# Kernel tuning notes

Hardware: AMD Instinct MI355X
Metric: run time of the kernel (lower is better)

Reference implementation:

```python
import jax, jax.numpy as jnp
import numpy as np

K = 16            # top-k negatives kept per row
TEMP = 0.01       # softmax temperature
V = 0.95          # geometric decay base
NEG_FILL = -1e9   # masks out same-class entries before topk (never selected since k << #negatives)


def _l2norm(x):
    # torch F.normalize: x / max(||x||, eps)
    n = jnp.linalg.norm(x, axis=-1, keepdims=True)
    return x / jnp.maximum(n, 1e-12)


def setup_inputs() -> dict:
    key = jax.random.key(0)
    k1, k2, k3 = jax.random.split(key, 3)
    feature = jax.random.normal(k1, (4096, 128), dtype=jnp.float32)
    negative_features = jax.random.normal(k2, (4, 4096, 128), dtype=jnp.float32)
    target = jax.random.randint(k3, (4096,), 0, 4)
    return {"feature": feature, "target": target,
            "negative_features": negative_features, "idx": 0}


def reference(feature, target, negative_features, idx):
    J = negative_features.shape[0]
    f = _l2norm(feature)                       # [n, d]
    negs = _l2norm(negative_features)          # [J, n, d]
    # cosine similarity for every negative set: [J, n, n]
    sims = jnp.einsum('nd,jmd->jnm', f, negs)
    # same-class mask, applied only to the idx-th set
    same = target[:, None] == target[None, :]  # [n, n]
    sims = sims.at[idx].set(jnp.where(same, NEG_FILL, sims[idx]))
    # per-row top-k over the last (candidate) dim: [J, n, K]
    top, _ = jax.lax.top_k(sims, K)
    logits = jnp.transpose(top, (1, 0, 2)) / TEMP   # [n, J, K]
    p = jax.nn.softmax(logits, axis=1)
    logp = jax.nn.log_softmax(logits, axis=1)
    ent = jnp.sum(p * logp, axis=1)                 # [n, K]
    decay = V ** jnp.arange(K, dtype=jnp.float32)
    decay = decay / jnp.sum(decay)                  # L1-normalized, matches F.normalize(p=1)
    loss = jnp.mean(jnp.sum(ent * decay, axis=1)) + jnp.log(jnp.float32(J))
    return loss
```

## Files before the change

kernel.cpp:

```cpp
#include <hip/hip_runtime.h>
#include <hip/hip_bf16.h>
#include <math.h>

#define N 4096
#define D 128
#define NJ 4
#define KTOP 16
#define CSPLIT 2

typedef __attribute__((ext_vector_type(8))) short bf16x8;
typedef __attribute__((ext_vector_type(4))) float f32x4;


__device__ __forceinline__ void bitonic_sort16_desc(float* a) {
    #pragma unroll
    for (int k = 2; k <= 16; k <<= 1) {
        #pragma unroll
        for (int jj = k >> 1; jj > 0; jj >>= 1) {
            #pragma unroll
            for (int i = 0; i < 16; i++) {
                int l = i ^ jj;
                if (l > i) {
                    bool up = ((i & k) == 0);
                    float x = a[i], y = a[l];
                    float mx = fmaxf(x, y), mn = fminf(x, y);
                    a[i] = up ? mx : mn;
                    a[l] = up ? mn : mx;
                }
            }
        }
    }
}

__device__ __forceinline__ void bitonic_clean16_desc(float* a) {
    #pragma unroll
    for (int jj = 8; jj > 0; jj >>= 1) {
        #pragma unroll
        for (int i = 0; i < 16; i++) {
            int l = i ^ jj;
            if (l > i) {
                float x = a[i], y = a[l];
                a[i] = fmaxf(x, y);
                a[l] = fminf(x, y);
            }
        }
    }
}

__global__ __launch_bounds__(256) void neguni_prep(
    const float* __restrict__ feat, const float* __restrict__ negs,
    unsigned short* __restrict__ fh, unsigned short* __restrict__ gh)
{
    const int w    = threadIdx.x >> 6;
    const int lane = threadIdx.x & 63;
    const int p    = lane & 15;
    const int rr   = lane >> 4;
    const int row  = blockIdx.x * 16 + w * 4 + rr;

    const float* src = (row < N) ? (feat + (size_t)row * D)
                                 : (negs + (size_t)(row - N) * D);
    float4 v0 = ((const float4*)src)[p * 2];
    float4 v1 = ((const float4*)src)[p * 2 + 1];
    float ss = v0.x*v0.x + v0.y*v0.y + v0.z*v0.z + v0.w*v0.w
             + v1.x*v1.x + v1.y*v1.y + v1.z*v1.z + v1.w*v1.w;
    ss += __shfl_xor(ss, 1, 64);
    ss += __shfl_xor(ss, 2, 64);
    ss += __shfl_xor(ss, 4, 64);
    ss += __shfl_xor(ss, 8, 64);
    const float inv = 1.0f / fmaxf(sqrtf(ss), 1e-12f);

    float f[8] = {v0.x, v0.y, v0.z, v0.w, v1.x, v1.y, v1.z, v1.w};
    unsigned int u[4];
    #pragma unroll
    for (int i = 0; i < 4; i++) {
        __hip_bfloat16 b0 = __float2bfloat16(f[2*i]   * inv);
        __hip_bfloat16 b1 = __float2bfloat16(f[2*i+1] * inv);
        u[i] = ((unsigned int)*(unsigned short*)&b1 << 16) | *(unsigned short*)&b0;
    }
    uint4 pk; pk.x = u[0]; pk.y = u[1]; pk.z = u[2]; pk.w = u[3];

    if (row < N) {
        *(uint4*)(fh + (size_t)row * D + p * 8) = pk;
    } else {
        const int rn  = row - N;
        const int j   = rn >> 12;
        const int rj  = rn & 4095;
        const int chg = rj >> 6;
        const int cl  = rj & 63;
        const int t   = cl >> 4;
        const int col = cl & 15;
        const int s   = p >> 2;
        const int q   = p & 3;
        *(uint4*)(gh + (size_t)j * N * D + (size_t)chg * 8192
                  + (s * 4 + t) * 512 + (q * 16 + col) * 8) = pk;
    }
}

__global__ __launch_bounds__(256) void neguni_main(
    const unsigned short* __restrict__ fh, const unsigned short* __restrict__ gh,
    const int* __restrict__ target, const int* __restrict__ idxp,
    float* __restrict__ topbuf)
{
    __shared__ float tops[4][16][17];

    const int tid   = threadIdx.x;
    const int w     = tid >> 6;
    const int lane  = tid & 63;
    const int col16 = lane & 15;
    const int quad  = lane >> 4;

    const int j   = blockIdx.x & 3;
    const int ft  = (blockIdx.x >> 2) & 255;
    const int cs  = blockIdx.x >> 10;
    const int r0  = ft * 16;
    const int c0  = cs * 2048 + w * 512;
    const int idx = idxp[0];
    const bool msk = (j == idx);

    bf16x8 bfr[4];
    {
        const unsigned short* fr = fh + (size_t)(r0 + col16) * D + quad * 8;
        bfr[0] = *(const bf16x8*)(fr);
        bfr[1] = *(const bf16x8*)(fr + 32);
        bfr[2] = *(const bf16x8*)(fr + 64);
        bfr[3] = *(const bf16x8*)(fr + 96);
    }
    const int rtg = target[r0 + col16];

    float lst[KTOP];

    const int chg0 = cs * 32 + w * 8;
    const unsigned short* ab0 = gh + (size_t)j * N * D + (size_t)chg0 * 8192 + lane * 8;

    #pragma unroll 1
    for (int ch = 0; ch < 8; ch++) {
        const unsigned short* ab = ab0 + (size_t)ch * 8192;

        f32x4 acc[4];
        #pragma unroll
        for (int t = 0; t < 4; t++) acc[t] = (f32x4){0.f, 0.f, 0.f, 0.f};

        #pragma unroll
        for (int s = 0; s < 4; s++) {
            #pragma unroll
            for (int t = 0; t < 4; t++) {
                bf16x8 a = *(const bf16x8*)(ab + (s * 4 + t) * 512);
                acc[t] = __builtin_amdgcn_mfma_f32_16x16x32_bf16(a, bfr[s], acc[t], 0, 0, 0);
            }
        }

        const int cbase = c0 + ch * 64;
        float s16[16];
        #pragma unroll
        for (int t = 0; t < 4; t++) {
            s16[t * 4 + 0] = acc[t][0];
            s16[t * 4 + 1] = acc[t][1];
            s16[t * 4 + 2] = acc[t][2];
            s16[t * 4 + 3] = acc[t][3];
        }
        if (msk) {
            #pragma unroll
            for (int t = 0; t < 4; t++) {
                int4 tc = *(const int4*)(target + cbase + t * 16 + quad * 4);
                if (tc.x == rtg) s16[t * 4 + 0] = -1e9f;
                if (tc.y == rtg) s16[t * 4 + 1] = -1e9f;
                if (tc.z == rtg) s16[t * 4 + 2] = -1e9f;
                if (tc.w == rtg) s16[t * 4 + 3] = -1e9f;
            }
        }

        bitonic_sort16_desc(s16);
        if (ch == 0) {
            #pragma unroll
            for (int i = 0; i < 16; i++) lst[i] = s16[i];
        } else {
            float mg[16];
            #pragma unroll
            for (int i = 0; i < 16; i++) mg[i] = fmaxf(lst[i], s16[15 - i]);
            bitonic_clean16_desc(mg);
            #pragma unroll
            for (int i = 0; i < 16; i++) lst[i] = mg[i];
        }
    }

    #pragma unroll
    for (int off = 16; off <= 32; off <<= 1) {
        float mg[16];
        #pragma unroll
        for (int i = 0; i < 16; i++)
            mg[i] = fmaxf(lst[i], __shfl_xor(lst[15 - i], off, 64));
        bitonic_clean16_desc(mg);
        #pragma unroll
        for (int i = 0; i < 16; i++) lst[i] = mg[i];
    }

    if (lane < 16) {
        #pragma unroll
        for (int i = 0; i < 16; i++) tops[w][lane][i] = lst[i];
        tops[w][lane][16] = -3.0e38f;
    }
    __syncthreads();

    if (tid < 16) {
        int i0 = 0, i1 = 0, i2 = 0, i3 = 0;
        float* outp = topbuf + (((size_t)j * N + r0 + tid) * CSPLIT + cs) * KTOP;
        #pragma unroll
        for (int k = 0; k < KTOP; k++) {
            float v0 = tops[0][tid][i0], v1 = tops[1][tid][i1];
            float v2 = tops[2][tid][i2], v3 = tops[3][tid][i3];
            float m01 = fmaxf(v0, v1), m23 = fmaxf(v2, v3);
            float mx  = fmaxf(m01, m23);
            if      (mx == v0) i0++;
            else if (mx == v1) i1++;
            else if (mx == v2) i2++;
            else               i3++;
            outp[k] = mx;
        }
    }
}

__global__ __launch_bounds__(256) void neguni_fin(
    const float* __restrict__ topbuf, float* __restrict__ out)
{
    __shared__ float buf[256][35];
    __shared__ float mm[64][65];
    __shared__ float red[4];

    const int t     = threadIdx.x;
    const int j     = t >> 6;
    const int row_l = t & 63;
    const int row   = blockIdx.x * 64 + row_l;

    const float4* src = (const float4*)(topbuf + ((size_t)j * N + row) * (CSPLIT * KTOP));
    #pragma unroll
    for (int q = 0; q < 8; q++) {
        float4 v = src[q];
        const int base = (q >> 2) * 17 + (q & 3) * 4;
        buf[t][base + 0] = v.x;
        buf[t][base + 1] = v.y;
        buf[t][base + 2] = v.z;
        buf[t][base + 3] = v.w;
    }
    buf[t][16] = -3.0e38f;
    buf[t][33] = -3.0e38f;

    {
        int ia = 0, ib = 17;
        #pragma unroll
        for (int k = 0; k < KTOP; k++) {
            float va = buf[t][ia], vb = buf[t][ib];
            bool ta = va >= vb;
            mm[row_l][k * 4 + j] = ta ? va : vb;
            if (ta) ia++; else ib++;
        }
    }
    __syncthreads();

    float val = 0.f;
    const float Ssum = (1.0f - powf(0.95f, 16.0f)) / 0.05f;
    #pragma unroll
    for (int i = 0; i < 4; i++) {
        const int idx = t + i * 256;
        const int rl  = idx & 63;
        const int k   = idx >> 6;
        float l0 = mm[rl][k * 4 + 0] * 100.0f;
        float l1 = mm[rl][k * 4 + 1] * 100.0f;
        float l2 = mm[rl][k * 4 + 2] * 100.0f;
        float l3 = mm[rl][k * 4 + 3] * 100.0f;
        float m  = fmaxf(fmaxf(l0, l1), fmaxf(l2, l3));
        float d0 = l0 - m, d1 = l1 - m, d2 = l2 - m, d3 = l3 - m;
        float e0 = expf(d0), e1 = expf(d1), e2 = expf(d2), e3 = expf(d3);
        float s  = e0 + e1 + e2 + e3;
        float ent = (e0 * d0 + e1 * d1 + e2 * d2 + e3 * d3) / s - logf(s);
        val += ent * powf(0.95f, (float)k);
    }
    val *= 1.0f / (Ssum * (float)N);

    #pragma unroll
    for (int off = 32; off > 0; off >>= 1) val += __shfl_xor(val, off, 64);
    if ((t & 63) == 0) red[t >> 6] = val;
    __syncthreads();
    if (t == 0) atomicAdd(out, red[0] + red[1] + red[2] + red[3]);
    if (blockIdx.x == 0 && t == 0) atomicAdd(out, logf(4.0f));
}

extern "C" void kernel_launch(void* const* d_in, const int* in_sizes, int n_in,
                              void* d_out, int out_size, void* d_ws, size_t ws_size,
                              hipStream_t stream) {
    const float* feat   = (const float*)d_in[0];
    const int*   target = (const int*)d_in[1];
    const float* negs   = (const float*)d_in[2];
    const int*   idxp   = (const int*)d_in[3];
    float* out = (float*)d_out;

    unsigned short* fh = (unsigned short*)d_ws;
    unsigned short* gh = fh + (size_t)N * D;
    float* topbuf      = (float*)(gh + (size_t)NJ * N * D);

    hipMemsetAsync(out, 0, sizeof(float), stream);
    neguni_prep<<<dim3((N + NJ * N) / 16), dim3(256), 0, stream>>>(feat, negs, fh, gh);
    neguni_main<<<dim3(NJ * (N / 16) * CSPLIT), dim3(256), 0, stream>>>(fh, gh, target, idxp, topbuf);
    neguni_fin<<<dim3(N / 64), dim3(256), 0, stream>>>(topbuf, out);
}
```

Measured before the change: 133.4 us.

## Prefetch next chunk during sort, use sorting network, shrink finalize blocks

The main kernel now software-pipelines the chunk loop. It loads the next 64-column chunk's bf16 operands into registers before sorting and merging the current chunk, then runs the MFMAs, with a sched_barrier to keep the loads early. The 16-element bitonic sort with direction selects is replaced by a fixed compare-exchange sorting network with fewer comparators. The finalize kernel is resized to 64-thread blocks over 16 rows, drops the cross-wave shared reduction, and uses fast exp/log intrinsics and precomputed constants. The extra 16 prefetch registers raise register pressure and may lower occupancy.

New measurement: 141.6 us. 1.06x slower.

```diff
diff --git a/kernel.cpp b/kernel.cpp
--- a/kernel.cpp
+++ b/kernel.cpp
@@ -12,24 +12,27 @@
 typedef __attribute__((ext_vector_type(4))) float f32x4;
 
 
-__device__ __forceinline__ void bitonic_sort16_desc(float* a) {
-    #pragma unroll
-    for (int k = 2; k <= 16; k <<= 1) {
-        #pragma unroll
-        for (int jj = k >> 1; jj > 0; jj >>= 1) {
-            #pragma unroll
-            for (int i = 0; i < 16; i++) {
-                int l = i ^ jj;
-                if (l > i) {
-                    bool up = ((i & k) == 0);
-                    float x = a[i], y = a[l];
-                    float mx = fmaxf(x, y), mn = fminf(x, y);
-                    a[i] = up ? mx : mn;
-                    a[l] = up ? mn : mx;
-                }
-            }
-        }
-    }
+__device__ __forceinline__ void ce_desc(float* a, int i, int l) {
+    float x = a[i], y = a[l];
+    a[i] = fmaxf(x, y);
+    a[l] = fminf(x, y);
+}
+
+__device__ __forceinline__ void sort16_desc(float* a) {
+    ce_desc(a,0,1);  ce_desc(a,2,3);  ce_desc(a,0,2);  ce_desc(a,1,3);  ce_desc(a,1,2);
+    ce_desc(a,4,5);  ce_desc(a,6,7);  ce_desc(a,4,6);  ce_desc(a,5,7);  ce_desc(a,5,6);
+    ce_desc(a,0,4);  ce_desc(a,2,6);  ce_desc(a,2,4);  ce_desc(a,1,5);  ce_desc(a,3,7);
+    ce_desc(a,3,5);  ce_desc(a,1,2);  ce_desc(a,3,4);  ce_desc(a,5,6);
+    ce_desc(a,8,9);  ce_desc(a,10,11); ce_desc(a,8,10); ce_desc(a,9,11); ce_desc(a,9,10);
+    ce_desc(a,12,13); ce_desc(a,14,15); ce_desc(a,12,14); ce_desc(a,13,15); ce_desc(a,13,14);
+    ce_desc(a,8,12); ce_desc(a,10,14); ce_desc(a,10,12); ce_desc(a,9,13); ce_desc(a,11,15);
+    ce_desc(a,11,13); ce_desc(a,9,10); ce_desc(a,11,12); ce_desc(a,13,14);
+    ce_desc(a,0,8);  ce_desc(a,4,12); ce_desc(a,4,8);  ce_desc(a,2,10); ce_desc(a,6,14);
+    ce_desc(a,6,10); ce_desc(a,2,4);  ce_desc(a,6,8);  ce_desc(a,10,12);
+    ce_desc(a,1,9);  ce_desc(a,5,13); ce_desc(a,5,9);  ce_desc(a,3,11); ce_desc(a,7,15);
+    ce_desc(a,7,11); ce_desc(a,3,5);  ce_desc(a,7,9);  ce_desc(a,11,13);
+    ce_desc(a,1,2);  ce_desc(a,3,4);  ce_desc(a,5,6);  ce_desc(a,7,8);  ce_desc(a,9,10);
+    ce_desc(a,11,12); ce_desc(a,13,14);
 }
 
 __device__ __forceinline__ void bitonic_clean16_desc(float* a) {
@@ -127,27 +130,35 @@
     }
     const int rtg = target[r0 + col16];
 
-    float lst[KTOP];
-
     const int chg0 = cs * 32 + w * 8;
     const unsigned short* ab0 = gh + (size_t)j * N * D + (size_t)chg0 * 8192 + lane * 8;
 
+    float lst[KTOP];
+    f32x4 acc[4];
+
+    {
+        bf16x8 fA[16];
+        #pragma unroll
+        for (int u = 0; u < 16; u++) fA[u] = *(const bf16x8*)(ab0 + u * 512);
+        #pragma unroll
+        for (int t = 0; t < 4; t++) acc[t] = (f32x4){0.f, 0.f, 0.f, 0.f};
+        #pragma unroll
+        for (int s = 0; s < 4; s++) {
+            #pragma unroll
+            for (int t = 0; t < 4; t++)
+                acc[t] = __builtin_amdgcn_mfma_f32_16x16x32_bf16(fA[s * 4 + t], bfr[s], acc[t], 0, 0, 0);
+        }
+    }
+
     #pragma unroll 1
-    for (int ch = 0; ch < 8; ch++) {
-        const unsigned short* ab = ab0 + (size_t)ch * 8192;
-
-        f32x4 acc[4];
-        #pragma unroll
-        for (int t = 0; t < 4; t++) acc[t] = (f32x4){0.f, 0.f, 0.f, 0.f};
-
-        #pragma unroll
-        for (int s = 0; s < 4; s++) {
-            #pragma unroll
-            for (int t = 0; t < 4; t++) {
-                bf16x8 a = *(const bf16x8*)(ab + (s * 4 + t) * 512);
-                acc[t] = __builtin_amdgcn_mfma_f32_16x16x32_bf16(a, bfr[s], acc[t], 0, 0, 0);
-            }
-        }
+    for (int ch = 0; ch < 7; ch++) {
+        bf16x8 fB[16];
+        {
+            const unsigned short* ab = ab0 + (size_t)(ch + 1) * 8192;
+            #pragma unroll
+            for (int u = 0; u < 16; u++) fB[u] = *(const bf16x8*)(ab + u * 512);
+        }
+        __builtin_amdgcn_sched_barrier(0);
 
         const int cbase = c0 + ch * 64;
         float s16[16];
@@ -169,7 +180,7 @@
             }
         }
 
-        bitonic_sort16_desc(s16);
+        sort16_desc(s16);
         if (ch == 0) {
             #pragma unroll
             for (int i = 0; i < 16; i++) lst[i] = s16[i];
@@ -181,6 +192,44 @@
             #pragma unroll
             for (int i = 0; i < 16; i++) lst[i] = mg[i];
         }
+
+        #pragma unroll
+        for (int t = 0; t < 4; t++) acc[t] = (f32x4){0.f, 0.f, 0.f, 0.f};
+        #pragma unroll
+        for (int s = 0; s < 4; s++) {
+            #pragma unroll
+            for (int t = 0; t < 4; t++)
+                acc[t] = __builtin_amdgcn_mfma_f32_16x16x32_bf16(fB[s * 4 + t], bfr[s], acc[t], 0, 0, 0);
+        }
+    }
+
+    {
+        const int cbase = c0 + 7 * 64;
+        float s16[16];
+        #pragma unroll
+        for (int t = 0; t < 4; t++) {
+            s16[t * 4 + 0] = acc[t][0];
+            s16[t * 4 + 1] = acc[t][1];
+            s16[t * 4 + 2] = acc[t][2];
+            s16[t * 4 + 3] = acc[t][3];
+        }
+        if (msk) {
+            #pragma unroll
+            for (int t = 0; t < 4; t++) {
+                int4 tc = *(const int4*)(target + cbase + t * 16 + quad * 4);
+                if (tc.x == rtg) s16[t * 4 + 0] = -1e9f;
+                if (tc.y == rtg) s16[t * 4 + 1] = -1e9f;
+                if (tc.z == rtg) s16[t * 4 + 2] = -1e9f;
+                if (tc.w == rtg) s16[t * 4 + 3] = -1e9f;
+            }
+        }
+        sort16_desc(s16);
+        float mg[16];
+        #pragma unroll
+        for (int i = 0; i < 16; i++) mg[i] = fmaxf(lst[i], s16[15 - i]);
+        bitonic_clean16_desc(mg);
+        #pragma unroll
+        for (int i = 0; i < 16; i++) lst[i] = mg[i];
     }
 
     #pragma unroll
@@ -219,17 +268,16 @@
     }
 }
 
-__global__ __launch_bounds__(256) void neguni_fin(
+__global__ __launch_bounds__(64) void neguni_fin(
     const float* __restrict__ topbuf, float* __restrict__ out)
 {
-    __shared__ float buf[256][35];
-    __shared__ float mm[64][65];
-    __shared__ float red[4];
+    __shared__ float buf[64][35];
+    __shared__ float mm[16][65];
 
     const int t     = threadIdx.x;
-    const int j     = t >> 6;
-    const int row_l = t & 63;
-    const int row   = blockIdx.x * 64 + row_l;
+    const int j     = t >> 4;
+    const int row_l = t & 15;
+    const int row   = blockIdx.x * 16 + row_l;
 
     const float4* src = (const float4*)(topbuf + ((size_t)j * N + row) * (CSPLIT * KTOP));
     #pragma unroll
@@ -257,31 +305,31 @@
     __syncthreads();
 
     float val = 0.f;
-    const float Ssum = (1.0f - powf(0.95f, 16.0f)) / 0.05f;
     #pragma unroll
     for (int i = 0; i < 4; i++) {
-        const int idx = t + i * 256;
-        const int rl  = idx & 63;
-        const int k   = idx >> 6;
+        const int idx2 = t + i * 64;
+        const int rl   = idx2 & 15;
+        const int k    = idx2 >> 4;
         float l0 = mm[rl][k * 4 + 0] * 100.0f;
         float l1 = mm[rl][k * 4 + 1] * 100.0f;
         float l2 = mm[rl][k * 4 + 2] * 100.0f;
         float l3 = mm[rl][k * 4 + 3] * 100.0f;
         float m  = fmaxf(fmaxf(l0, l1), fmaxf(l2, l3));
         float d0 = l0 - m, d1 = l1 - m, d2 = l2 - m, d3 = l3 - m;
-        float e0 = expf(d0), e1 = expf(d1), e2 = expf(d2), e3 = expf(d3);
+        float e0 = __expf(d0), e1 = __expf(d1), e2 = __expf(d2), e3 = __expf(d3);
         float s  = e0 + e1 + e2 + e3;
-        float ent = (e0 * d0 + e1 * d1 + e2 * d2 + e3 * d3) / s - logf(s);
-        val += ent * powf(0.95f, (float)k);
-    }
-    val *= 1.0f / (Ssum * (float)N);
+        float ent = (e0 * d0 + e1 * d1 + e2 * d2 + e3 * d3) / s - __logf(s);
+        float dk  = __expf(-0.05129329439f * (float)k);
+        val += ent * dk;
+    }
+    val *= (1.0f / (11.1974666f * (float)N));
 
     #pragma unroll
     for (int off = 32; off > 0; off >>= 1) val += __shfl_xor(val, off, 64);
-    if ((t & 63) == 0) red[t >> 6] = val;
-    __syncthreads();
-    if (t == 0) atomicAdd(out, red[0] + red[1] + red[2] + red[3]);
-    if (blockIdx.x == 0 && t == 0) atomicAdd(out, logf(4.0f));
+    if (t == 0) {
+        atomicAdd(out, val);
+        if (blockIdx.x == 0) atomicAdd(out, 1.38629436112f);
+    }
 }
 
 extern "C" void kernel_launch(void* const* d_in, const int* in_sizes, int n_in,
@@ -300,5 +348,5 @@
     hipMemsetAsync(out, 0, sizeof(float), stream);
     neguni_prep<<<dim3((N + NJ * N) / 16), dim3(256), 0, stream>>>(feat, negs, fh, gh);
     neguni_main<<<dim3(NJ * (N / 16) * CSPLIT), dim3(256), 0, stream>>>(fh, gh, target, idxp, topbuf);
-    neguni_fin<<<dim3(N / 64), dim3(256), 0, stream>>>(topbuf, out);
-}
+    neguni_fin<<<dim3(N / 16), dim3(64), 0, stream>>>(topbuf, out);
+}
```
